# Kernel tuning notes

Measured on AMD Instinct MI355X. Metric: run time of the kernel, lower is better.

## Reference

```python
import jax, jax.numpy as jnp
import numpy as np

HID = 256
NL = 4
NC = 5
SPACE = 16


def _grid_sample(feat, grid):
    # feat [B,C,H,W]; grid [B,Hg,Wg,2] in [-1,1]; bilinear, align_corners=True, zeros padding
    B, C, H, W = feat.shape
    x = (grid[..., 0] + 1.0) * 0.5 * (W - 1)
    y = (grid[..., 1] + 1.0) * 0.5 * (H - 1)
    x0f = jnp.floor(x)
    y0f = jnp.floor(y)
    wx1 = x - x0f
    wy1 = y - y0f

    def corner(yf, xf, wgt):
        valid = (xf >= 0) & (xf <= W - 1) & (yf >= 0) & (yf <= H - 1)
        xi = jnp.clip(xf, 0, W - 1).astype(jnp.int32)
        yi = jnp.clip(yf, 0, H - 1).astype(jnp.int32)
        v = jax.vmap(lambda f, yy, xx: f[:, yy, xx])(feat, yi, xi)  # [B,C,Hg,Wg]
        return v * (wgt * valid.astype(feat.dtype))[:, None]

    return (corner(y0f, x0f, (1 - wy1) * (1 - wx1))
            + corner(y0f, x0f + 1, (1 - wy1) * wx1)
            + corner(y0f + 1, x0f, wy1 * (1 - wx1))
            + corner(y0f + 1, x0f + 1, wy1 * wx1))


def _conv(x, w, b, pad):
    y = jax.lax.conv_general_dilated(x, w, (1, 1), ((pad, pad), (pad, pad)),
                                     dimension_numbers=('NCHW', 'OIHW', 'NCHW'))
    return y + b[None, :, None, None]


def _resize_ac(x, oh, ow):
    # bilinear resize with align_corners=True
    B, C, H, W = x.shape
    ys = jnp.linspace(0.0, H - 1.0, oh)
    xs = jnp.linspace(0.0, W - 1.0, ow)
    y0 = jnp.floor(ys).astype(jnp.int32)
    y1 = jnp.minimum(y0 + 1, H - 1)
    x0 = jnp.floor(xs).astype(jnp.int32)
    x1 = jnp.minimum(x0 + 1, W - 1)
    wy = (ys - y0)[None, None, :, None]
    wx = (xs - x0)[None, None, None, :]
    top = x[:, :, y0, :] * (1 - wy) + x[:, :, y1, :] * wy
    return top[:, :, :, x0] * (1 - wx) + top[:, :, :, x1] * wx


def _mlp(x, w1, b1, w2, b2):
    # 2-layer MLP, dropout is identity at inference
    return jax.nn.relu(x @ w1 + b1) @ w2 + b2


def setup_inputs() -> dict:
    key = jax.random.key(0)
    ks = jax.random.split(key, 16)
    B, H, W = 8, 512, 512

    def rn(k, shape, s=0.02):
        return jax.random.normal(k, shape, jnp.float32) * s

    return {
        'images': jax.random.normal(ks[0], (B, 3, H, W), jnp.float32),
        'feat0': jax.random.normal(ks[1], (B, HID, 128, 128), jnp.float32),
        'feat1': jax.random.normal(ks[2], (B, HID, 64, 64), jnp.float32),
        'feat2': jax.random.normal(ks[3], (B, HID, 32, 32), jnp.float32),
        'feat3': jax.random.normal(ks[4], (B, HID, 16, 16), jnp.float32),
        'mask_feat': jax.random.normal(ks[5], (B, HID, 128, 128), jnp.float32),
        'o': jax.random.normal(ks[6], (B, 16, 16, 768), jnp.float32),
        'dw1': rn(ks[7], (768, HID)), 'db1': jnp.zeros((HID,), jnp.float32),
        'dw2': rn(ks[8], (HID, 8)), 'db2': jnp.zeros((8,), jnp.float32),
        'cw1': rn(ks[9], (HID, HID)), 'cb1': jnp.zeros((HID,), jnp.float32),
        'cw2': rn(ks[10], (HID, NC + 1)), 'cb2': jnp.zeros((NC + 1,), jnp.float32),
        'conv_w': rn(ks[11], (HID, HID * NL, 3, 3)), 'conv_b': jnp.zeros((HID,), jnp.float32),
        'mw1': rn(ks[12], (HID, HID, 3, 3)), 'mb1': jnp.zeros((HID,), jnp.float32),
        'bn_g': jnp.ones((HID,), jnp.float32), 'bn_b': jnp.zeros((HID,), jnp.float32),
        'bn_m': jnp.zeros((HID,), jnp.float32), 'bn_v': jnp.ones((HID,), jnp.float32),
        'mw2': rn(ks[13], (1, HID, 1, 1)), 'mb2': jnp.zeros((1,), jnp.float32),
    }


def reference(images, feat0, feat1, feat2, feat3, mask_feat, o,
              dw1, db1, dw2, db2, cw1, cb1, cw2, cb2, conv_w, conv_b,
              mw1, mb1, bn_g, bn_b, bn_m, bn_v, mw2, mb2):
    B, _, H, W = images.shape
    ny = int(np.ceil(H / SPACE))
    nx = int(np.ceil(W / SPACE))
    # AnchorPoints: meshgrid 'xy', scaled by space, shifted by half-cell origin
    gx, gy = jnp.meshgrid(jnp.arange(nx, dtype=jnp.float32), jnp.arange(ny, dtype=jnp.float32))
    origin = jnp.array([(W % SPACE) or SPACE, (H % SPACE) or SPACE], jnp.float32) / 2
    anchors = jnp.stack([gx, gy], -1) * SPACE + origin  # [ny,nx,2] (x,y)

    # learned offsets: MLP then pixel-shuffle style 16x16x8 -> 32x32x2
    d = _mlp(o, dw1, db1, dw2, db2)  # [B,16,16,8]
    d = d.reshape(B, 16, 16, 2, 2, 2).transpose(0, 1, 3, 2, 4, 5).reshape(B, 32, 32, 2)
    prop = anchors[None] + d  # deformed proposals [B,32,32,2]

    feats = [feat0, feat1, feat2, feat3]
    strides = [4, 8, 16, 32]
    rois = []
    for f, s in zip(feats, strides):
        fh, fw = f.shape[2], f.shape[3]
        grid = 2.0 * prop / s / jnp.array([fw, fh], jnp.float32) - 1.0
        rois.append(_grid_sample(f, grid))
    roi = jnp.concatenate(rois, 1)  # [B, HID*NL, 32, 32]
    roi = _conv(roi, conv_w, conv_b, 1).transpose(0, 2, 3, 1)  # [B,32,32,HID]
    logits = _mlp(roi, cw1, cb1, cw2, cb2)  # [B,32,32,NC+1]

    # mask head: conv3x3 -> BN(eval) -> ReLU -> conv1x1(pad=1) -> bilinear upsample (align_corners=True)
    m = _conv(mask_feat, mw1, mb1, 1)
    m = m * (bn_g * jax.lax.rsqrt(bn_v + 1e-5))[None, :, None, None] \
        + (bn_b - bn_m * bn_g * jax.lax.rsqrt(bn_v + 1e-5))[None, :, None, None]
    m = jax.nn.relu(m)
    m = _conv(m, mw2, mb2, 1)  # 1x1 conv with padding=1 -> [B,1,130,130] (as in source)
    masks = _resize_ac(m, H, W)  # [B,1,H,W]

    return (prop.reshape(B, -1, 2), logits.reshape(B, -1, NC + 1), masks)
```

## Files before the change

### kernel.cpp

```cpp
#include <hip/hip_runtime.h>
#include <hip/hip_bf16.h>
#include <cstdint>
#include <cstddef>

using bf16x8 = __attribute__((ext_vector_type(8))) short;
using f32x4  = __attribute__((ext_vector_type(4))) float;

static constexpr size_t PART_OFF = 4194308;
static constexpr size_t WT_OFF   = 16777220;
static constexpr size_t WTR_SH   = (size_t)294912 * 8;
static constexpr size_t WTM_SH   = (size_t)73728 * 8;
static constexpr size_t M2P_OFF  = WT_OFF + (WTR_SH + WTM_SH) / 2;

__device__ __forceinline__ uint32_t pk2(float a, float b) {
  __hip_bfloat162 h = __float22bfloat162_rn(make_float2(a, b));
  union { __hip_bfloat162 h; uint32_t u; } c; c.h = h;
  return c.u;
}

__device__ __forceinline__ void gld16(const void* g, void* l) {
  __builtin_amdgcn_global_load_lds(
      (const __attribute__((address_space(1))) void*)g,
      (__attribute__((address_space(3))) void*)l, 16, 0, 0);
}

__global__ __launch_bounds__(256) void k_prep_w(
    const float* __restrict__ conv_w, const float* __restrict__ mw1,
    short* __restrict__ wTr, short* __restrict__ wTm, float* __restrict__ zp) {
  __shared__ float sm[16 * 292];
  int t = threadIdx.x;
  int bid = blockIdx.x;
  if (bid == 0 && t < 4) zp[t] = 0.f;
  bool is_m = (bid >= 512);
  int b2 = is_m ? (bid - 512) : bid;
  int kidx = is_m ? (b2 & 7) : (b2 & 31);
  int cog  = is_m ? (b2 >> 3) : (b2 >> 5);
  const float* src = is_m ? mw1 : conv_w;
  short* dst = is_m ? wTm : wTr;
  int CI = is_m ? 256 : 1024;
  int ci0 = kidx * 32;
  int co0 = cog * 16;
  for (int e = t; e < 4608; e += 256) {
    int row = e / 288, pos = e - row * 288;
    sm[row * 292 + pos] = src[((size_t)(co0 + row) * CI + ci0) * 9 + pos];
  }
  __syncthreads();
  int nb = cog >> 3, cofrag = cog & 7;
  for (int e = t; e < 576; e += 256) {
    int tap = e >> 6, kg = (e >> 4) & 3, lr = e & 15;
    float v[8];
#pragma unroll
    for (int j = 0; j < 8; ++j) v[j] = sm[lr * 292 + (kg * 8 + j) * 9 + tap];
    uint4 pk = make_uint4(pk2(v[0], v[1]), pk2(v[2], v[3]),
                          pk2(v[4], v[5]), pk2(v[6], v[7]));
    size_t chunk = ((size_t)(kidx * 2 + nb) * 9 + tap) * 512
                 + cofrag * 64 + kg * 16 + lr;
    *(uint4*)&dst[chunk * 8] = pk;
  }
}

__global__ __launch_bounds__(256) void k_prop(
    const float* __restrict__ o,
    const float* __restrict__ dw1, const float* __restrict__ db1,
    const float* __restrict__ dw2, const float* __restrict__ db2,
    float* __restrict__ prop) {
  __shared__ float o_lds[4 * 768];
  __shared__ float h_lds[4 * 256];
  int t = threadIdx.x;
  int bid = blockIdx.x;
  int b = bid >> 6;
  int rem = bid & 63;
  int i = rem >> 2;
  int j0 = (rem & 3) * 4;
  const float* obase = o + ((size_t)(b * 16 + i) * 16 + j0) * 768;
  for (int e = t; e < 4 * 768; e += 256) o_lds[e] = obase[e];
  __syncthreads();
  float h0 = 0.f, h1 = 0.f, h2 = 0.f, h3 = 0.f;
  for (int k = 0; k < 768; ++k) {
    float w = dw1[k * 256 + t];
    h0 = fmaf(o_lds[k], w, h0);
    h1 = fmaf(o_lds[768 + k], w, h1);
    h2 = fmaf(o_lds[1536 + k], w, h2);
    h3 = fmaf(o_lds[2304 + k], w, h3);
  }
  float bb = db1[t];
  h_lds[t]        = fmaxf(h0 + bb, 0.f);
  h_lds[256 + t]  = fmaxf(h1 + bb, 0.f);
  h_lds[512 + t]  = fmaxf(h2 + bb, 0.f);
  h_lds[768 + t]  = fmaxf(h3 + bb, 0.f);
  __syncthreads();
  if (t < 32) {
    int pos = t >> 3;
    int c   = t & 7;
    float acc = db2[c];
    const float* hp = h_lds + pos * 256;
    for (int k = 0; k < 256; ++k) acc = fmaf(hp[k], dw2[k * 8 + c], acc);
    int p = c >> 2, q = (c >> 1) & 1, cc = c & 1;
    int row = 2 * i + p;
    int col = 2 * (j0 + pos) + q;
    float anchor = (cc == 0) ? ((float)col * 16.f + 8.f) : ((float)row * 16.f + 8.f);
    prop[((size_t)(b * 32 + row) * 32 + col) * 2 + cc] = anchor + acc;
  }
}

__global__ __launch_bounds__(256) void k_sample(
    const float* __restrict__ f0, const float* __restrict__ f1,
    const float* __restrict__ f2, const float* __restrict__ f3,
    const float* __restrict__ prop, uint4* __restrict__ bfR) {
  int py = blockIdx.x;
  int l  = blockIdx.y;
  int b  = blockIdx.z;
  int t  = threadIdx.x;
  int xq = t & 31;
  int cq = t >> 5;
  const float* f = (l == 0) ? f0 : (l == 1) ? f1 : (l == 2) ? f2 : f3;
  int fsz = 128 >> l;
  float s = (float)(4 << l);

  size_t pidx = ((size_t)b * 32 + py) * 32 + xq;
  float px = prop[pidx * 2 + 0];
  float pv = prop[pidx * 2 + 1];
  float gx = 2.f * px / s / (float)fsz - 1.f;
  float gy = 2.f * pv / s / (float)fsz - 1.f;
  float x = (gx + 1.f) * 0.5f * (float)(fsz - 1);
  float y = (gy + 1.f) * 0.5f * (float)(fsz - 1);
  float x0f = floorf(x), y0f = floorf(y);
  float wx1 = x - x0f, wy1 = y - y0f;

  int off[4];
  float wgt[4];
#pragma unroll
  for (int cy = 0; cy < 2; ++cy) {
#pragma unroll
    for (int cx = 0; cx < 2; ++cx) {
      float xf = x0f + (float)cx;
      float yf = y0f + (float)cy;
      float w = (cy ? wy1 : (1.f - wy1)) * (cx ? wx1 : (1.f - wx1));
      bool valid = (xf >= 0.f) && (xf <= (float)(fsz - 1)) &&
                   (yf >= 0.f) && (yf <= (float)(fsz - 1));
      int xi = (int)fminf(fmaxf(xf, 0.f), (float)(fsz - 1));
      int yi = (int)fminf(fmaxf(yf, 0.f), (float)(fsz - 1));
      off[cy * 2 + cx] = yi * fsz + xi;
      wgt[cy * 2 + cx] = valid ? w : 0.f;
    }
  }
  const float* fb = f + (size_t)b * 256 * fsz * fsz;
#pragma unroll
  for (int i = 0; i < 4; ++i) {
    int cgl = i * 8 + cq;
    float v[8];
#pragma unroll
    for (int j = 0; j < 8; ++j) {
      const float* fc = fb + (size_t)(cgl * 8 + j) * fsz * fsz;
      v[j] = wgt[0] * fc[off[0]] + wgt[1] * fc[off[1]] +
             wgt[2] * fc[off[2]] + wgt[3] * fc[off[3]];
    }
    bfR[(((size_t)b * 128 + l * 32 + cgl) * 32 + py) * 32 + xq] =
        make_uint4(pk2(v[0], v[1]), pk2(v[2], v[3]),
                   pk2(v[4], v[5]), pk2(v[6], v[7]));
  }
}

__global__ __launch_bounds__(256) void k_cvt(const float* __restrict__ mf,
                                             uint4* __restrict__ bfA) {
  int d = blockIdx.x * 256 + threadIdx.x;
  int x = d & 127, y = (d >> 7) & 127, cg = (d >> 14) & 31, b = d >> 19;
  const float* src = mf + (((size_t)(b * 256 + cg * 8)) << 14) + (y << 7) + x;
  float v[8];
#pragma unroll
  for (int j = 0; j < 8; ++j) v[j] = src[(size_t)j << 14];
  bfA[d] = make_uint4(pk2(v[0], v[1]), pk2(v[2], v[3]),
                      pk2(v[4], v[5]), pk2(v[6], v[7]));
}

__global__ __launch_bounds__(512, 2) void k_roi_mfma(
    const uint4* __restrict__ bfR, const short* __restrict__ wTr,
    float* __restrict__ part) {
  __shared__ __align__(16) short A_s[2][1408 * 8];
  __shared__ __align__(16) short B_s[4608 * 8];
  int t = threadIdx.x;
  int lane = t & 63, wv = t >> 6, wm = wv >> 1, wn = wv & 1;
  int kg = lane >> 4, lr = lane & 15;
  int bid = blockIdx.x;
  int nb = bid & 1;
  int mi = (bid >> 1) & 31;
  int b = mi >> 2, yt = mi & 3;
  int ks = bid >> 6;

  f32x4 acc[4][4];
#pragma unroll
  for (int m = 0; m < 4; ++m)
#pragma unroll
    for (int n = 0; n < 4; ++n) acc[m][n] = {0.f, 0.f, 0.f, 0.f};

  auto issue_A = [&](int buf, int kc) {
#pragma unroll
    for (int i = 0; i < 3; ++i) {
      int wq = wv + 8 * i;
      if (wq < 22) {
        int c = wq * 64 + lane;
        int pxi = c >> 2, slot = c & 3;
        int r = pxi / 34;
        int x = pxi - r * 34 - 1;
        int y = yt * 8 + r - 1;
        int cg4 = slot ^ ((pxi >> 1) & 3);
        bool ok = (r < 10) && (x >= 0) && (x < 32) && (y >= 0) && (y < 32);
        long chunk = ok ? (long)((((b * 128 + ks * 32 + kc * 4 + cg4) * 32 + y) * 32) + x)
                        : -1L;
        gld16(bfR + chunk, &A_s[buf][wq * 512]);
      }
    }
  };
  auto issue_h1 = [&](int kc) {
    const short* s = wTr + ((size_t)((ks * 8 + kc) * 2 + nb) * 4608) * 8;
    for (int w = wv; w < 40; w += 8)
      gld16(s + ((size_t)w * 64 + lane) * 8, &B_s[w * 512]);
  };
  auto issue_h2 = [&](int kc) {
    const short* s = wTr + (((size_t)((ks * 8 + kc) * 2 + nb) * 4608 + 2560)) * 8;
    for (int w = wv; w < 32; w += 8)
      gld16(s + ((size_t)w * 64 + lane) * 8, &B_s[2560 * 8 + w * 512]);
  };

#define ROI_TAPS(T0, T1)                                                          \
  {                                                                               \
    _Pragma("unroll")                                                             \
    for (int tap = (T0); tap < (T1); ++tap) {                                     \
      int ky = tap / 3, kx = tap - ky * 3;                                        \
      bf16x8 bfr[4];                                                              \
      _Pragma("unroll")                                                           \
      for (int n = 0; n < 4; ++n)                                                 \
        bfr[n] = *(const bf16x8*)&B_s[((((tap * 8 + wn * 4 + n) * 4 + kg) * 16)   \
                                       + lr) * 8];                                \
      _Pragma("unroll")                                                           \
      for (int m = 0; m < 4; ++m) {                                               \
        int pb = wm * 64 + m * 16;                                                \
        int px = ((pb >> 5) + ky) * 34 + (pb & 31) + lr + kx;                     \
        bf16x8 af = *(const bf16x8*)&As[(px * 4 + ((kg ^ (px >> 1)) & 3)) * 8];   \
        _Pragma("unroll")                                                         \
        for (int n = 0; n < 4; ++n)                                               \
          acc[m][n] = __builtin_amdgcn_mfma_f32_16x16x32_bf16(af, bfr[n],         \
                                                              acc[m][n], 0, 0, 0);\
      }                                                                           \
    }                                                                             \
  }

  issue_h1(0);
  issue_A(0, 0);
  __syncthreads();

  for (int kc = 0; kc < 8; ++kc) {
    int buf = kc & 1;
    const short* As = A_s[buf];
    if (kc < 7) issue_A(buf ^ 1, kc + 1);
    issue_h2(kc);
    ROI_TAPS(0, 5);
    __syncthreads();
    if (kc < 7) issue_h1(kc + 1);
    ROI_TAPS(5, 9);
    __syncthreads();
  }
#pragma unroll
  for (int m = 0; m < 4; ++m)
#pragma unroll
    for (int r = 0; r < 4; ++r) {
      int p = wm * 64 + m * 16 + kg * 4 + r;
      int y = yt * 8 + (p >> 5), x = p & 31;
      float* dst = part + (size_t)ks * 2097152 + (((size_t)b * 32 + y) * 32 + x) * 256
                        + nb * 128 + wn * 64 + lr;
#pragma unroll
      for (int n = 0; n < 4; ++n) dst[n * 16] = acc[m][n][r];
    }
}

__global__ __launch_bounds__(256) void k_mlp(
    const float* __restrict__ part, const float* __restrict__ conv_b,
    const float* __restrict__ cw1, const float* __restrict__ cb1,
    const float* __restrict__ cw2, const float* __restrict__ cb2,
    float* __restrict__ logits) {
  __shared__ float v[1024];
  __shared__ float h[1024];
  int t = threadIdx.x;
  size_t base = (size_t)blockIdx.x * 1024;
  const size_t CH = (size_t)8192 * 256;
  for (int e = t; e < 1024; e += 256) {
    float s = part[base + e] + part[CH + base + e] +
              part[2 * CH + base + e] + part[3 * CH + base + e];
    v[e] = s + conv_b[e & 255];
  }
  __syncthreads();
  float a0 = cb1[t], a1 = a0, a2 = a0, a3 = a0;
  for (int k = 0; k < 256; ++k) {
    float w = cw1[k * 256 + t];
    a0 = fmaf(v[k], w, a0);
    a1 = fmaf(v[256 + k], w, a1);
    a2 = fmaf(v[512 + k], w, a2);
    a3 = fmaf(v[768 + k], w, a3);
  }
  h[t]       = fmaxf(a0, 0.f);
  h[256 + t] = fmaxf(a1, 0.f);
  h[512 + t] = fmaxf(a2, 0.f);
  h[768 + t] = fmaxf(a3, 0.f);
  __syncthreads();
  if (t < 24) {
    int pos = t / 6, c = t - 6 * pos;
    float acc = cb2[c];
    const float* hp = h + pos * 256;
    for (int k = 0; k < 256; ++k) acc = fmaf(hp[k], cw2[k * 6 + c], acc);
    logits[((size_t)blockIdx.x * 4 + pos) * 6 + c] = acc;
  }
}

__global__ __launch_bounds__(512, 2) void k_mask_mfma(
    const uint4* __restrict__ bfA, const short* __restrict__ wTm,
    const float* __restrict__ mb1,
    const float* __restrict__ bn_g, const float* __restrict__ bn_b,
    const float* __restrict__ bn_m, const float* __restrict__ bn_v,
    const float* __restrict__ mw2, float* __restrict__ m2p) {
  __shared__ __align__(16) short A_s[2][2112 * 8];
  __shared__ __align__(16) short B_s[4608 * 8];
  int t = threadIdx.x;
  int lane = t & 63, wv = t >> 6, wm = wv >> 1, wn = wv & 1;
  int kg = lane >> 4, lr = lane & 15;
  int bid = blockIdx.x;
  int nb = bid & 1;
  int tile = bid >> 1;
  int b = tile >> 6, yt = tile & 63;

  f32x4 acc[4][4];
#pragma unroll
  for (int m = 0; m < 4; ++m)
#pragma unroll
    for (int n = 0; n < 4; ++n) acc[m][n] = {0.f, 0.f, 0.f, 0.f};

  auto issue_A = [&](int buf, int kc) {
#pragma unroll
    for (int i = 0; i < 5; ++i) {
      int wq = wv + 8 * i;
      if (wq < 33) {
        int c = wq * 64 + lane;
        int pxi = c >> 2, slot = c & 3;
        int r = pxi / 130;
        int x = pxi - r * 130 - 1;
        int y = 2 * yt + r - 1;
        int cg4 = slot ^ ((pxi >> 1) & 3);
        bool ok = (r < 4) && (x >= 0) && (x < 128) && (y >= 0) && (y < 128);
        long chunk = ok ? (long)((((b * 32 + kc * 4 + cg4) * 128 + y) * 128) + x)
                        : -1L;
        gld16(bfA + chunk, &A_s[buf][wq * 512]);
      }
    }
  };
  auto issue_h1 = [&](int kc) {
    const short* s = wTm + ((size_t)(kc * 2 + nb) * 4608) * 8;
    for (int w = wv; w < 40; w += 8)
      gld16(s + ((size_t)w * 64 + lane) * 8, &B_s[w * 512]);
  };
  auto issue_h2 = [&](int kc) {
    const short* s = wTm + (((size_t)(kc * 2 + nb) * 4608 + 2560)) * 8;
    for (int w = wv; w < 32; w += 8)
      gld16(s + ((size_t)w * 64 + lane) * 8, &B_s[2560 * 8 + w * 512]);
  };

#define MSK_TAPS(T0, T1)                                                          \
  {                                                                               \
    _Pragma("unroll")                                                             \
    for (int tap = (T0); tap < (T1); ++tap) {                                     \
      int ky = tap / 3, kx = tap - ky * 3;                                        \
      bf16x8 bfr[4];                                                              \
      _Pragma("unroll")                                                           \
      for (int n = 0; n < 4; ++n)                                                 \
        bfr[n] = *(const bf16x8*)&B_s[((((tap * 8 + wn * 4 + n) * 4 + kg) * 16)   \
                                       + lr) * 8];                                \
      _Pragma("unroll")                                                           \
      for (int m = 0; m < 4; ++m) {                                               \
        int px = ((wm >> 1) + ky) * 130 + (wm & 1) * 64 + m * 16 + lr + kx;       \
        bf16x8 af = *(const bf16x8*)&As[(px * 4 + ((kg ^ (px >> 1)) & 3)) * 8];   \
        _Pragma("unroll")                                                         \
        for (int n = 0; n < 4; ++n)                                               \
          acc[m][n] = __builtin_amdgcn_mfma_f32_16x16x32_bf16(af, bfr[n],         \
                                                              acc[m][n], 0, 0, 0);\
      }                                                                           \
    }                                                                             \
  }

  issue_h1(0);
  issue_A(0, 0);
  __syncthreads();

  for (int kc = 0; kc < 8; ++kc) {
    int buf = kc & 1;
    const short* As = A_s[buf];
    if (kc < 7) issue_A(buf ^ 1, kc + 1);
    issue_h2(kc);
    MSK_TAPS(0, 5);
    __syncthreads();
    if (kc < 7) issue_h1(kc + 1);
    MSK_TAPS(5, 9);
    __syncthreads();
  }

  float sc[4], sh[4], w2v[4], b1[4];
#pragma unroll
  for (int n = 0; n < 4; ++n) {
    int co = nb * 128 + wn * 64 + n * 16 + lr;
    float s = bn_g[co] * rsqrtf(bn_v[co] + 1e-5f);
    sc[n] = s;
    sh[n] = bn_b[co] - bn_m[co] * s;
    b1[n] = mb1[co];
    w2v[n] = mw2[co];
  }
  float* red = (float*)&A_s[0][0];
#pragma unroll
  for (int m = 0; m < 4; ++m)
#pragma unroll
    for (int r = 0; r < 4; ++r) {
      int p = (wm >> 1) * 128 + (wm & 1) * 64 + m * 16 + kg * 4 + r;
      float s = 0.f;
#pragma unroll
      for (int n = 0; n < 4; ++n) {
        float z = fmaf(acc[m][n][r] + b1[n], sc[n], sh[n]);
        s = fmaf(w2v[n], fmaxf(z, 0.f), s);
      }
      red[p * 32 + wn * 16 + lr] = s;
    }
  __syncthreads();
  if (t < 256) {
    float s = 0.f;
#pragma unroll
    for (int q = 0; q < 32; ++q) s += red[t * 32 + q];
    int y = 2 * yt + (t >> 7);
    int x = t & 127;
    m2p[(size_t)nb * 131072 + ((size_t)b * 128 + y) * 128 + x] = s;
  }
}

__global__ __launch_bounds__(256) void k_resize(const float* __restrict__ m2p,
                                                const float* __restrict__ mb2,
                                                float* __restrict__ masks) {
  int idx = blockIdx.x * 256 + threadIdx.x;
  int b = idx >> 18;
  int rem = idx & 262143;
  int y = rem >> 9;
  int x = rem & 511;
  const float SC = 129.0f / 511.0f;
  float sy = (float)y * SC;
  float sx = (float)x * SC;
  float y0f = floorf(sy), x0f = floorf(sx);
  int y0 = (int)y0f, x0 = (int)x0f;
  int y1 = min(y0 + 1, 129), x1 = min(x0 + 1, 129);
  float wy = sy - y0f, wx = sx - x0f;
  float base = mb2[0];
  const float* p0 = m2p + (size_t)b * 16384;
  const float* p1 = m2p + 131072 + (size_t)b * 16384;

  auto corner = [&](int yy, int xx) -> float {
    if (yy >= 1 && yy <= 128 && xx >= 1 && xx <= 128) {
      int o2 = (yy - 1) * 128 + (xx - 1);
      return base + p0[o2] + p1[o2];
    }
    return base;
  };
  float tv = corner(y0, x0) * (1.f - wx) + corner(y0, x1) * wx;
  float bv = corner(y1, x0) * (1.f - wx) + corner(y1, x1) * wx;
  masks[idx] = tv * (1.f - wy) + bv * wy;
}

extern "C" void kernel_launch(void* const* d_in, const int* in_sizes, int n_in,
                              void* d_out, int out_size, void* d_ws, size_t ws_size,
                              hipStream_t stream) {
  (void)in_sizes; (void)n_in; (void)out_size; (void)ws_size;
  const float* f0        = (const float*)d_in[1];
  const float* f1        = (const float*)d_in[2];
  const float* f2        = (const float*)d_in[3];
  const float* f3        = (const float*)d_in[4];
  const float* mask_feat = (const float*)d_in[5];
  const float* o         = (const float*)d_in[6];
  const float* dw1       = (const float*)d_in[7];
  const float* db1       = (const float*)d_in[8];
  const float* dw2       = (const float*)d_in[9];
  const float* db2       = (const float*)d_in[10];
  const float* cw1       = (const float*)d_in[11];
  const float* cb1       = (const float*)d_in[12];
  const float* cw2       = (const float*)d_in[13];
  const float* cb2       = (const float*)d_in[14];
  const float* conv_w    = (const float*)d_in[15];
  const float* conv_b    = (const float*)d_in[16];
  const float* mw1       = (const float*)d_in[17];
  const float* mb1       = (const float*)d_in[18];
  const float* bn_g      = (const float*)d_in[19];
  const float* bn_b      = (const float*)d_in[20];
  const float* bn_m      = (const float*)d_in[21];
  const float* bn_v      = (const float*)d_in[22];
  const float* mw2       = (const float*)d_in[23];
  const float* mb2       = (const float*)d_in[24];

  float* ws   = (float*)d_ws;
  uint4* bf   = (uint4*)(ws + 4);
  float* part = ws + PART_OFF;
  short* wTr  = (short*)(ws + WT_OFF);
  short* wTm  = wTr + WTR_SH;
  float* m2p  = ws + M2P_OFF;

  float* out_prop   = (float*)d_out;
  float* out_logits = out_prop + (size_t)8 * 1024 * 2;
  float* out_masks  = out_logits + (size_t)8 * 1024 * 6;

  hipLaunchKernelGGL(k_prep_w, dim3(640), dim3(256), 0, stream,
                     conv_w, mw1, wTr, wTm, ws);
  hipLaunchKernelGGL(k_prop, dim3(512), dim3(256), 0, stream,
                     o, dw1, db1, dw2, db2, out_prop);
  hipLaunchKernelGGL(k_sample, dim3(32, 4, 8), dim3(256), 0, stream,
                     f0, f1, f2, f3, out_prop, bf);
  hipLaunchKernelGGL(k_roi_mfma, dim3(256), dim3(512), 0, stream,
                     bf, wTr, part);
  hipLaunchKernelGGL(k_mlp, dim3(2048), dim3(256), 0, stream,
                     part, conv_b, cw1, cb1, cw2, cb2, out_logits);
  hipLaunchKernelGGL(k_cvt, dim3(16384), dim3(256), 0, stream,
                     mask_feat, bf);
  hipLaunchKernelGGL(k_mask_mfma, dim3(1024), dim3(512), 0, stream,
                     bf, wTm, mb1, bn_g, bn_b, bn_m, bn_v, mw2, m2p);
  hipLaunchKernelGGL(k_resize, dim3(8192), dim3(256), 0, stream,
                     m2p, mb2, out_masks);
}
```

Measured before the change: 352.1 us.

## Use partial vmcnt barriers, precomputed load addresses and setprio in conv pipelines

In the ROI and mask 3x3 conv kernels, the mid-iteration barrier now waits only for the older loads (s_waitcnt vmcnt(N) before s_barrier). This lets the prefetch of the next A tile stay in flight across the barrier instead of draining it. Per-lane global and LDS addresses for the A and B loads are computed once before the loop and advanced by a fixed stride, and the last k-chunk is peeled out. MFMA sections are wrapped in s_setprio to favour math waves. The risk is that correctness depends on the exact vmcnt counts matching how many loads each wave issues, and the extra address registers raise register pressure.

Result: no change. 350.8 us (-0.4%).

```diff
diff --git a/kernel.cpp b/kernel.cpp
--- a/kernel.cpp
+++ b/kernel.cpp
@@ -23,6 +23,12 @@
       (const __attribute__((address_space(1))) void*)g,
       (__attribute__((address_space(3))) void*)l, 16, 0, 0);
 }
+
+#define CBAR(N) do { \
+    asm volatile("s_waitcnt vmcnt(" #N ")" ::: "memory"); \
+    __builtin_amdgcn_sched_barrier(0); \
+    __builtin_amdgcn_s_barrier(); \
+    __builtin_amdgcn_sched_barrier(0); } while (0)
 
 __global__ __launch_bounds__(256) void k_prep_w(
     const float* __restrict__ conv_w, const float* __restrict__ mw1,
@@ -193,34 +199,62 @@
 #pragma unroll
     for (int n = 0; n < 4; ++n) acc[m][n] = {0.f, 0.f, 0.f, 0.f};
 
-  auto issue_A = [&](int buf, int kc) {
-#pragma unroll
-    for (int i = 0; i < 3; ++i) {
-      int wq = wv + 8 * i;
-      if (wq < 22) {
-        int c = wq * 64 + lane;
-        int pxi = c >> 2, slot = c & 3;
-        int r = pxi / 34;
-        int x = pxi - r * 34 - 1;
-        int y = yt * 8 + r - 1;
-        int cg4 = slot ^ ((pxi >> 1) & 3);
-        bool ok = (r < 10) && (x >= 0) && (x < 32) && (y >= 0) && (y < 32);
-        long chunk = ok ? (long)((((b * 128 + ks * 32 + kc * 4 + cg4) * 32 + y) * 32) + x)
-                        : -1L;
-        gld16(bfR + chunk, &A_s[buf][wq * 512]);
-      }
-    }
-  };
-  auto issue_h1 = [&](int kc) {
-    const short* s = wTr + ((size_t)((ks * 8 + kc) * 2 + nb) * 4608) * 8;
-    for (int w = wv; w < 40; w += 8)
-      gld16(s + ((size_t)w * 64 + lane) * 8, &B_s[w * 512]);
-  };
-  auto issue_h2 = [&](int kc) {
-    const short* s = wTr + (((size_t)((ks * 8 + kc) * 2 + nb) * 4608 + 2560)) * 8;
-    for (int w = wv; w < 32; w += 8)
-      gld16(s + ((size_t)w * 64 + lane) * 8, &B_s[2560 * 8 + w * 512]);
-  };
+  const uint4* aptr[3];
+  int astep[3], aldst[3];
+  bool aon[3];
+#pragma unroll
+  for (int i = 0; i < 3; ++i) {
+    int wq = wv + 8 * i;
+    aon[i] = wq < 22;
+    int c = wq * 64 + lane;
+    int pxi = c >> 2, slot = c & 3;
+    int r = pxi / 34;
+    int x = pxi - r * 34 - 1;
+    int y = yt * 8 + r - 1;
+    int cg4 = slot ^ ((pxi >> 1) & 3);
+    bool ok = (r < 10) && (x >= 0) && (x < 32) && (y >= 0) && (y < 32);
+    long chunk = ok ? (long)((((b * 128 + ks * 32 + cg4) * 32 + y) * 32) + x) : -1L;
+    aptr[i] = bfR + chunk;
+    astep[i] = ok ? 4096 : 0;
+    aldst[i] = wq * 512;
+  }
+  int bg1[5], bl1[5], bg2[4], bl2[4];
+#pragma unroll
+  for (int j = 0; j < 5; ++j) {
+    int w = wv + 8 * j;
+    bg1[j] = (w * 64 + lane) * 8;
+    bl1[j] = w * 512;
+  }
+#pragma unroll
+  for (int j = 0; j < 4; ++j) {
+    int w = wv + 8 * j;
+    bg2[j] = (2560 + w * 64 + lane) * 8;
+    bl2[j] = 20480 + w * 512;
+  }
+  const size_t BKC = (size_t)4608 * 8;
+  const short* bbase = wTr + ((size_t)(ks * 8) * 2 + nb) * BKC;
+
+#define ROI_ISSUE_A(BUF)                                         \
+  {                                                              \
+    _Pragma("unroll")                                            \
+    for (int i = 0; i < 3; ++i)                                  \
+      if (aon[i]) {                                              \
+        gld16(aptr[i], &A_s[BUF][aldst[i]]);                     \
+        aptr[i] += astep[i];                                     \
+      }                                                          \
+  }
+#define ROI_ISSUE_H1(KC)                                         \
+  {                                                              \
+    const short* bk = bbase + (size_t)(KC) * 2 * BKC;            \
+    _Pragma("unroll")                                            \
+    for (int j = 0; j < 5; ++j) gld16(bk + bg1[j], &B_s[bl1[j]]);\
+  }
+#define ROI_ISSUE_H2(KC)                                         \
+  {                                                              \
+    const short* bk = bbase + (size_t)(KC) * 2 * BKC;            \
+    _Pragma("unroll")                                            \
+    for (int j = 0; j < 4; ++j) gld16(bk + bg2[j], &B_s[bl2[j]]);\
+  }
 
 #define ROI_TAPS(T0, T1)                                                          \
   {                                                                               \
@@ -245,20 +279,35 @@
     }                                                                             \
   }
 
-  issue_h1(0);
-  issue_A(0, 0);
-  __syncthreads();
-
-  for (int kc = 0; kc < 8; ++kc) {
+  ROI_ISSUE_H1(0);
+  ROI_ISSUE_A(0);
+  __syncthreads();
+
+  for (int kc = 0; kc < 7; ++kc) {
     int buf = kc & 1;
     const short* As = A_s[buf];
-    if (kc < 7) issue_A(buf ^ 1, kc + 1);
-    issue_h2(kc);
+    ROI_ISSUE_H2(kc);
+    ROI_ISSUE_A(buf ^ 1);
+    __builtin_amdgcn_s_setprio(1);
     ROI_TAPS(0, 5);
-    __syncthreads();
-    if (kc < 7) issue_h1(kc + 1);
+    __builtin_amdgcn_s_setprio(0);
+    CBAR(2);
+    ROI_ISSUE_H1(kc + 1);
+    __builtin_amdgcn_s_setprio(1);
     ROI_TAPS(5, 9);
-    __syncthreads();
+    __builtin_amdgcn_s_setprio(0);
+    CBAR(0);
+  }
+  {
+    const short* As = A_s[1];
+    ROI_ISSUE_H2(7);
+    __builtin_amdgcn_s_setprio(1);
+    ROI_TAPS(0, 5);
+    __builtin_amdgcn_s_setprio(0);
+    CBAR(0);
+    __builtin_amdgcn_s_setprio(1);
+    ROI_TAPS(5, 9);
+    __builtin_amdgcn_s_setprio(0);
   }
 #pragma unroll
   for (int m = 0; m < 4; ++m)
@@ -333,34 +382,62 @@
 #pragma unroll
     for (int n = 0; n < 4; ++n) acc[m][n] = {0.f, 0.f, 0.f, 0.f};
 
-  auto issue_A = [&](int buf, int kc) {
-#pragma unroll
-    for (int i = 0; i < 5; ++i) {
-      int wq = wv + 8 * i;
-      if (wq < 33) {
-        int c = wq * 64 + lane;
-        int pxi = c >> 2, slot = c & 3;
-        int r = pxi / 130;
-        int x = pxi - r * 130 - 1;
-        int y = 2 * yt + r - 1;
-        int cg4 = slot ^ ((pxi >> 1) & 3);
-        bool ok = (r < 4) && (x >= 0) && (x < 128) && (y >= 0) && (y < 128);
-        long chunk = ok ? (long)((((b * 32 + kc * 4 + cg4) * 128 + y) * 128) + x)
-                        : -1L;
-        gld16(bfA + chunk, &A_s[buf][wq * 512]);
-      }
-    }
-  };
-  auto issue_h1 = [&](int kc) {
-    const short* s = wTm + ((size_t)(kc * 2 + nb) * 4608) * 8;
-    for (int w = wv; w < 40; w += 8)
-      gld16(s + ((size_t)w * 64 + lane) * 8, &B_s[w * 512]);
-  };
-  auto issue_h2 = [&](int kc) {
-    const short* s = wTm + (((size_t)(kc * 2 + nb) * 4608 + 2560)) * 8;
-    for (int w = wv; w < 32; w += 8)
-      gld16(s + ((size_t)w * 64 + lane) * 8, &B_s[2560 * 8 + w * 512]);
-  };
+  const uint4* aptr[5];
+  int astep[5], aldst[5];
+  bool aon[5];
+#pragma unroll
+  for (int i = 0; i < 5; ++i) {
+    int wq = wv + 8 * i;
+    aon[i] = wq < 33;
+    int c = wq * 64 + lane;
+    int pxi = c >> 2, slot = c & 3;
+    int r = pxi / 130;
+    int x = pxi - r * 130 - 1;
+    int y = 2 * yt + r - 1;
+    int cg4 = slot ^ ((pxi >> 1) & 3);
+    bool ok = (r < 4) && (x >= 0) && (x < 128) && (y >= 0) && (y < 128);
+    long chunk = ok ? (long)((((b * 32 + cg4) * 128 + y) * 128) + x) : -1L;
+    aptr[i] = bfA + chunk;
+    astep[i] = ok ? 65536 : 0;
+    aldst[i] = wq * 512;
+  }
+  int bg1[5], bl1[5], bg2[4], bl2[4];
+#pragma unroll
+  for (int j = 0; j < 5; ++j) {
+    int w = wv + 8 * j;
+    bg1[j] = (w * 64 + lane) * 8;
+    bl1[j] = w * 512;
+  }
+#pragma unroll
+  for (int j = 0; j < 4; ++j) {
+    int w = wv + 8 * j;
+    bg2[j] = (2560 + w * 64 + lane) * 8;
+    bl2[j] = 20480 + w * 512;
+  }
+  const size_t BKC = (size_t)4608 * 8;
+  const short* bbase = wTm + (size_t)nb * BKC;
+
+#define MSK_ISSUE_A(BUF)                                         \
+  {                                                              \
+    _Pragma("unroll")                                            \
+    for (int i = 0; i < 5; ++i)                                  \
+      if (aon[i]) {                                              \
+        gld16(aptr[i], &A_s[BUF][aldst[i]]);                     \
+        aptr[i] += astep[i];                                     \
+      }                                                          \
+  }
+#define MSK_ISSUE_H1(KC)                                         \
+  {                                                              \
+    const short* bk = bbase + (size_t)(KC) * 2 * BKC;            \
+    _Pragma("unroll")                                            \
+    for (int j = 0; j < 5; ++j) gld16(bk + bg1[j], &B_s[bl1[j]]);\
+  }
+#define MSK_ISSUE_H2(KC)                                         \
+  {                                                              \
+    const short* bk = bbase + (size_t)(KC) * 2 * BKC;            \
+    _Pragma("unroll")                                            \
+    for (int j = 0; j < 4; ++j) gld16(bk + bg2[j], &B_s[bl2[j]]);\
+  }
 
 #define MSK_TAPS(T0, T1)                                                          \
   {                                                                               \
@@ -384,20 +461,35 @@
     }                                                                             \
   }
 
-  issue_h1(0);
-  issue_A(0, 0);
-  __syncthreads();
-
-  for (int kc = 0; kc < 8; ++kc) {
+  MSK_ISSUE_H1(0);
+  MSK_ISSUE_A(0);
+  __syncthreads();
+
+  for (int kc = 0; kc < 7; ++kc) {
     int buf = kc & 1;
     const short* As = A_s[buf];
-    if (kc < 7) issue_A(buf ^ 1, kc + 1);
-    issue_h2(kc);
+    MSK_ISSUE_H2(kc);
+    MSK_ISSUE_A(buf ^ 1);
+    __builtin_amdgcn_s_setprio(1);
     MSK_TAPS(0, 5);
-    __syncthreads();
-    if (kc < 7) issue_h1(kc + 1);
+    __builtin_amdgcn_s_setprio(0);
+    CBAR(4);
+    MSK_ISSUE_H1(kc + 1);
+    __builtin_amdgcn_s_setprio(1);
     MSK_TAPS(5, 9);
-    __syncthreads();
+    __builtin_amdgcn_s_setprio(0);
+    CBAR(0);
+  }
+  {
+    const short* As = A_s[1];
+    MSK_ISSUE_H2(7);
+    __builtin_amdgcn_s_setprio(1);
+    MSK_TAPS(0, 5);
+    __builtin_amdgcn_s_setprio(0);
+    CBAR(0);
+    __builtin_amdgcn_s_setprio(1);
+    MSK_TAPS(5, 9);
+    __builtin_amdgcn_s_setprio(0);
   }
 
   float sc[4], sh[4], w2v[4], b1[4];
```
